# Performance work log

Hardware: AMD Instinct MI355X
Metric: run time of the kernel (lower is better)

The kernel has to match this reference:

```python
import jax, jax.numpy as jnp
import numpy as np

K = 3            # kernel_size
KK = K * K       # 9 neighbors per pixel
DILATIONS = [1, 2, 3]
NUM_HEADS = 3


def conv2d(x, w, b, dilation, padding):
    # x: [B,Cin,H,W], w: [Cout,Cin,kh,kw]
    out = jax.lax.conv_general_dilated(
        x, w, window_strides=(1, 1),
        padding=((padding, padding), (padding, padding)),
        rhs_dilation=(dilation, dilation),
        dimension_numbers=('NCHW', 'OIHW', 'NCHW'))
    if b is not None:
        out = out + b[None, :, None, None]
    return out


def unfold3(x, dil):
    # nn.Unfold(kernel=3, dilation=dil, padding=dil, stride=1): [B,C,H,W] -> [B, C*9, H*W]
    B, C, H, W = x.shape
    xp = jnp.pad(x, ((0, 0), (0, 0), (dil, dil), (dil, dil)))
    patches = [xp[:, :, i * dil:i * dil + H, j * dil:j * dil + W]
               for i in range(K) for j in range(K)]
    p = jnp.stack(patches, axis=2)          # [B,C,9,H,W] (channel-major like torch unfold)
    return p.reshape(B, C * KK, H * W)


def bilinear_sample(x, py, px):
    # x: [B,C,H,W]; py, px: [B,K2,H,W] float sample coords -> [B,C,K2,H,W]
    B, C, H, W = x.shape
    K2 = py.shape[1]
    y0 = jnp.floor(py); x0 = jnp.floor(px)
    wy = py - y0; wx = px - x0
    x_flat = x.reshape(B, C, H * W)

    def gather(yi, xi):
        yii = yi.astype(jnp.int32); xii = xi.astype(jnp.int32)
        valid = (yii >= 0) & (yii < H) & (xii >= 0) & (xii < W)
        yc = jnp.clip(yii, 0, H - 1); xc = jnp.clip(xii, 0, W - 1)
        idx = (yc * W + xc).reshape(B, -1)                       # [B, K2*H*W]
        vals = jnp.take_along_axis(x_flat, idx[:, None, :], axis=2)
        vals = vals.reshape(B, C, K2, H, W)
        return vals * valid[:, None].astype(x.dtype)

    v00 = gather(y0, x0); v01 = gather(y0, x0 + 1)
    v10 = gather(y0 + 1, x0); v11 = gather(y0 + 1, x0 + 1)
    wy = wy[:, None]; wx = wx[:, None]
    return (v00 * (1 - wy) * (1 - wx) + v01 * (1 - wy) * wx
            + v10 * wy * (1 - wx) + v11 * wy * wx)


def deform_conv(x, offsets, w, b, dil):
    # torchvision DeformConv2d, stride 1, padding=dil, dilation=dil, kernel 3
    B, C, H, W = x.shape
    off = offsets.reshape(B, KK, 2, H, W)                 # [..., (dy,dx), ...]
    ky, kx = jnp.meshgrid(jnp.arange(K), jnp.arange(K), indexing='ij')
    base_dy = (ky.reshape(KK) * dil - dil).astype(x.dtype)
    base_dx = (kx.reshape(KK) * dil - dil).astype(x.dtype)
    hh = jnp.arange(H, dtype=x.dtype); ww = jnp.arange(W, dtype=x.dtype)
    py = hh[None, None, :, None] + base_dy[None, :, None, None] + off[:, :, 0]
    px = ww[None, None, None, :] + base_dx[None, :, None, None] + off[:, :, 1]
    sampled = bilinear_sample(x, py, px)                  # [B,C,9,H,W]
    out = jnp.einsum('bckhw,ock->bohw', sampled, w.reshape(w.shape[0], C, KK))
    return out + b[None, :, None, None]


def adda_attention(q, k, v, head_dim, dil, deform_params):
    # q,k,v: [B,d,H,W] (already stop-gradiented)
    B, d, H, W = q.shape
    scale = head_dim ** -0.5
    if dil != 1:
        ow, ob, dw, db = deform_params
        offsets = conv2d(k, ow, ob, dil, dil)             # [B, 2*9, H, W]
        k = deform_conv(k, offsets, dw, db, dil)
        v = deform_conv(v, offsets, dw, db, dil)
    ku = unfold3(k, dil)                                  # [B, d*9, HW]
    vu = unfold3(v, dil)
    g = d // head_dim
    HW = H * W
    qh = q.reshape(B, g, head_dim, 1, HW).transpose(0, 1, 4, 3, 2)   # [B,g,HW,1,hd]
    kh = ku.reshape(B, g, head_dim, KK, HW).transpose(0, 1, 4, 2, 3) # [B,g,HW,hd,9]
    vh = vu.reshape(B, g, head_dim, KK, HW).transpose(0, 1, 4, 3, 2) # [B,g,HW,9,hd]
    attn = jax.nn.softmax((qh @ kh) * scale, axis=-1)                # [B,g,HW,1,9]
    o = attn @ vh                                                    # [B,g,HW,1,hd]
    return o.transpose(0, 2, 1, 3, 4).reshape(B, H, W, d)


def setup_inputs() -> dict:
    key = jax.random.key(0)
    ks = jax.random.split(key, 16)
    B, H, W, C = 8, 64, 64, 192
    hd = C // NUM_HEADS  # 64 == C // num_dilation
    inp = {
        'x': jax.random.normal(ks[0], (B, H, W, C), jnp.float32),
        'qkv_w': jax.random.normal(ks[1], (3 * C, C, 1, 1), jnp.float32) * 0.05,
        'proj_w': jax.random.normal(ks[2], (C, C), jnp.float32) * 0.05,
        'proj_b': jnp.zeros((C,), jnp.float32),
        'off_w2': jax.random.normal(ks[3], (2 * KK, hd, K, K), jnp.float32) * 0.01,
        'off_b2': jnp.zeros((2 * KK,), jnp.float32),
        'def_w2': jax.random.normal(ks[4], (hd, hd, K, K), jnp.float32) * 0.05,
        'def_b2': jnp.zeros((hd,), jnp.float32),
        'off_w3': jax.random.normal(ks[5], (2 * KK, hd, K, K), jnp.float32) * 0.01,
        'off_b3': jnp.zeros((2 * KK,), jnp.float32),
        'def_w3': jax.random.normal(ks[6], (hd, hd, K, K), jnp.float32) * 0.05,
        'def_b3': jnp.zeros((hd,), jnp.float32),
    }
    return inp


def reference(x, qkv_w, proj_w, proj_b,
              off_w2, off_b2, def_w2, def_b2,
              off_w3, off_b3, def_w3, def_b3):
    B, H, W, C = x.shape
    nd = len(DILATIONS)
    d = C // nd
    hd = C // NUM_HEADS
    xc = x.transpose(0, 3, 1, 2)                              # [B,C,H,W]
    qkv = conv2d(xc, qkv_w, None, 1, 0)                       # [B,3C,H,W]
    qkv = qkv.reshape(B, 3, nd, d, H, W).transpose(2, 1, 0, 3, 4, 5)  # [nd,3,B,d,H,W]
    qkv = jax.lax.stop_gradient(qkv)                          # q,k,v are .detach()'d in torch
    deform = {2: (off_w2, off_b2, def_w2, def_b2),
              3: (off_w3, off_b3, def_w3, def_b3)}
    outs = []
    for i, dil in enumerate(DILATIONS):
        outs.append(adda_attention(qkv[i, 0], qkv[i, 1], qkv[i, 2],
                                   hd, dil, deform.get(dil)))
    out = jnp.stack(outs, axis=3).reshape(B, H, W, C)         # permute(1,2,3,0,4).reshape
    return out @ proj_w.T + proj_b
```

## Files before the change

kernel.cpp:

```cpp
#include <hip/hip_runtime.h>
#include <cmath>

#define kB    8
#define kH    64
#define kW    64
#define kHW   4096
#define kC    192
#define kD    64
#define kM    (kB * kHW)
#define kNQKV 576

typedef unsigned short ushort_t;
typedef __attribute__((ext_vector_type(8))) short  s8v;
typedef __attribute__((ext_vector_type(4))) float  f4v;

__device__ inline unsigned short bf16r(float f) {
    union { float f; unsigned u; } v; v.f = f;
    unsigned u = v.u + 0x7FFFu + ((v.u >> 16) & 1u);
    return (unsigned short)(u >> 16);
}
__device__ inline float bfu(short s) {
    union { unsigned u; float f; } v;
    v.u = ((unsigned)(unsigned short)s) << 16;
    return v.f;
}

__global__ void cvt_bf16(const float* __restrict__ src, unsigned* __restrict__ dst, int n2) {
    int i = blockIdx.x * 256 + threadIdx.x;
    if (i >= n2) return;
    float2 f = ((const float2*)src)[i];
    dst[i] = (unsigned)bf16r(f.x) | ((unsigned)bf16r(f.y) << 16);
}

__global__ void prep_all(const float* __restrict__ qkv_w,
                         const float* __restrict__ proj_w,
                         const float* __restrict__ def_w2,
                         const float* __restrict__ def_w3,
                         const float* __restrict__ off_w2,
                         const float* __restrict__ off_w3,
                         ushort_t* __restrict__ awb,
                         ushort_t* __restrict__ pwbp,
                         ushort_t* __restrict__ dwtb2,
                         ushort_t* __restrict__ dwtb3,
                         ushort_t* __restrict__ owtb2,
                         ushort_t* __restrict__ owtb3) {
    const int bid = blockIdx.x;
    const int tid = threadIdx.x;
    if (bid < 54) {
        int idx = bid * 256 + tid;
        if (idx >= 36 * 6 * 64) return;
        int lane = idx & 63;
        int kc   = (idx >> 6) % 6;
        int s    = idx / 384;
        int row  = s * 16 + (lane & 15);
        int k0   = kc * 32 + (lane >> 4) * 8;
        const float* src = qkv_w + (size_t)row * kC + k0;
        ushort_t* dst = awb + (size_t)idx * 8;
#pragma unroll
        for (int j = 0; j < 8; ++j) dst[j] = bf16r(src[j]);
    } else if (bid < 72) {
        int idx = (bid - 54) * 256 + tid;
        if (idx >= 12 * 6 * 64) return;
        int lane = idx & 63;
        int kc   = (idx >> 6) % 6;
        int s    = idx / 384;
        int row  = s * 16 + (lane & 15);
        int k0   = kc * 32 + (lane >> 4) * 8;
        const float* src = proj_w + (size_t)row * kC + k0;
        ushort_t* dst = pwbp + (size_t)idx * 8;
#pragma unroll
        for (int j = 0; j < 8; ++j) dst[j] = bf16r(src[j]);
    } else if (bid < 360) {
        const float* dw = (bid < 216) ? def_w2 : def_w3;
        ushort_t* dwtb  = (bid < 216) ? dwtb2 : dwtb3;
        int l = ((bid < 216) ? (bid - 72) : (bid - 216)) * 256 + tid;
        if (l >= kD * kD * 9) return;
        int o = l / 576;
        int c = (l / 9) % 64;
        int kk = l % 9;
        dwtb[(kk * 64 + o) * 64 + c] = bf16r(dw[l]);
    } else {
        const float* ow = (bid < 432) ? off_w2 : off_w3;
        ushort_t* owtb  = (bid < 432) ? owtb2 : owtb3;
        int l = ((bid < 432) ? (bid - 360) : (bid - 432)) * 256 + tid;
        if (l >= 9 * 32 * 64) return;
        int kk = l >> 11;
        int j  = (l >> 6) & 31;
        int c  = l & 63;
        owtb[l] = (j < 18) ? bf16r(ow[j * 576 + c * 9 + kk]) : (ushort_t)0;
    }
}

__global__ __launch_bounds__(256) void qkv_mfma3(const ushort_t* __restrict__ xb,
                                                 const ushort_t* __restrict__ awb,
                                                 ushort_t* __restrict__ qkvpx) {
    __shared__ ushort_t xs[64 * kC];

    const int tid = threadIdx.x;
    const int bx  = blockIdx.x;
    const int lb  = (bx & 7) * 64 + (bx >> 3);
    const int m0  = lb * 64;
    const int ty3 = blockIdx.y;

#pragma unroll
    for (int i = 0; i < 6; ++i) {
        int il = i * 256 + tid;
        int p  = il / 24;
        int cc = il % 24;
        uint4 v = *(const uint4*)(xb + (size_t)(m0 + p) * kC + cc * 8);
        int dst = p * 384 + ((cc * 16) ^ ((p & 7) << 4));
        *(uint4*)((char*)xs + dst) = v;
    }
    __syncthreads();

    const int lane = tid & 63;
    const int wave = tid >> 6;
    const int l15  = lane & 15;
    const int q    = lane >> 4;
    const int sbase = ty3 * 12 + wave * 3;

    f4v acc[3][4];
#pragma unroll
    for (int i = 0; i < 3; ++i)
#pragma unroll
        for (int m = 0; m < 4; ++m) acc[i][m] = (f4v){0.f, 0.f, 0.f, 0.f};

    const ushort_t* ap = awb + ((size_t)sbase * 6 * 64 + lane) * 8;

#pragma unroll
    for (int kc = 0; kc < 6; ++kc) {
        s8v bfr[4];
#pragma unroll
        for (int m = 0; m < 4; ++m) {
            int row = m * 16 + l15;
            int col = (kc * 64 + q * 16) ^ ((l15 & 7) << 4);
            bfr[m] = *(const s8v*)((const char*)xs + row * 384 + col);
        }
#pragma unroll
        for (int i = 0; i < 3; ++i) {
            s8v a = *(const s8v*)(ap + (size_t)(i * 6 + kc) * 64 * 8);
#pragma unroll
            for (int m = 0; m < 4; ++m)
                acc[i][m] = __builtin_amdgcn_mfma_f32_16x16x32_bf16(a, bfr[m], acc[i][m], 0, 0, 0);
        }
    }

#pragma unroll
    for (int i = 0; i < 3; ++i) {
        int s   = sbase + i;
        int ty  = s >> 2;
        int c64 = (s & 3) * 16 + q * 4;
        ushort_t* obase = qkvpx + (size_t)ty * kM * 64 + (size_t)m0 * 64 + c64;
#pragma unroll
        for (int m = 0; m < 4; ++m) {
            f4v v = acc[i][m];
            uint2 u;
            u.x = (unsigned)bf16r(v.x) | ((unsigned)bf16r(v.y) << 16);
            u.y = (unsigned)bf16r(v.z) | ((unsigned)bf16r(v.w) << 16);
            *(uint2*)(obase + (size_t)(m * 16 + l15) * 64) = u;
        }
    }
}

__global__ __launch_bounds__(256) void off_conv_mfma(const ushort_t* __restrict__ kpx,
                                                     const ushort_t* __restrict__ owtb,
                                                     const float* __restrict__ obias,
                                                     float* __restrict__ offb,
                                                     int dil) {
    const int lb = (blockIdx.x & 7) * 64 + (blockIdx.x >> 3);
    const int b = lb >> 6;
    const int y = lb & 63;
    const int tid  = threadIdx.x;
    const int lane = tid & 63;
    const int wave = tid >> 6;
    const int l15  = lane & 15;
    const int q    = lane >> 4;
    const int px   = wave * 16 + l15;

    const ushort_t* inpx = kpx + (size_t)b * kHW * 64 + q * 8;

    f4v acc[2];
    acc[0] = (f4v){0.f, 0.f, 0.f, 0.f};
    acc[1] = (f4v){0.f, 0.f, 0.f, 0.f};

#pragma unroll
    for (int kk = 0; kk < 9; ++kk) {
        const int yy = y + (kk / 3 - 1) * dil;
        const int xx = px + (kk % 3 - 1) * dil;
        const bool valid = (yy >= 0) & (yy < kH) & (xx >= 0) & (xx < kW);
        const size_t idx = valid ? (size_t)(yy * kW + xx) * 64 : 0;
        s8v a0 = *(const s8v*)(inpx + idx);
        s8v a1 = *(const s8v*)(inpx + idx + 32);
        if (!valid) {
            a0 = (s8v){0, 0, 0, 0, 0, 0, 0, 0};
            a1 = (s8v){0, 0, 0, 0, 0, 0, 0, 0};
        }
        const ushort_t* wb = owtb + (size_t)kk * 2048 + l15 * 64 + q * 8;
#pragma unroll
        for (int nbk = 0; nbk < 2; ++nbk) {
            s8v b0 = *(const s8v*)(wb + nbk * 1024);
            s8v b1 = *(const s8v*)(wb + nbk * 1024 + 32);
            acc[nbk] = __builtin_amdgcn_mfma_f32_16x16x32_bf16(a0, b0, acc[nbk], 0, 0, 0);
            acc[nbk] = __builtin_amdgcn_mfma_f32_16x16x32_bf16(a1, b1, acc[nbk], 0, 0, 0);
        }
    }
#pragma unroll
    for (int nbk = 0; nbk < 2; ++nbk) {
        int n = nbk * 16 + l15;
        if (n < 18) {
            float bias = obias[n];
            f4v v = acc[nbk];
            v.x += bias; v.y += bias; v.z += bias; v.w += bias;
            *(f4v*)&offb[((size_t)b * 18 + n) * kHW + y * kW + wave * 16 + q * 4] = v;
        }
    }
}

template<int DIL>
__global__ __launch_bounds__(512) void deform_lds(const ushort_t* __restrict__ kpx,
                                                  const ushort_t* __restrict__ vpx,
                                                  const float* __restrict__ offb,
                                                  const ushort_t* __restrict__ dwtb,
                                                  const float* __restrict__ db,
                                                  ushort_t* __restrict__ outkpx,
                                                  ushort_t* __restrict__ outvpx) {
    constexpr int NR = 2 * DIL + 4;
    __shared__ ushort_t kv[NR * 4096];
    __shared__ ushort_t wlds[9 * 4096];

    const int tid = threadIdx.x;
    const int bx  = blockIdx.x;
    const int lb  = (bx & 7) * 64 + (bx >> 3);
    const int t   = lb >> 8;
    const int b   = (lb >> 5) & 7;
    const int y0  = (lb & 31) * 2;
    const int wlo = y0 - DIL - 1;

    const ushort_t* inb = (t ? vpx : kpx) + (size_t)b * kHW * 64;
    ushort_t* outp = t ? outvpx : outkpx;

#pragma unroll
    for (int i = 0; i < 9; ++i) {
        int g = (i * 512 + tid) * 16;
        uint4 v = *(const uint4*)((const char*)dwtb + g);
        int row = (g >> 7) & 63;
        int dst = g ^ ((row & 7) << 4);
        *(uint4*)((char*)wlds + dst) = v;
    }
#pragma unroll
    for (int r = 0; r < NR; ++r) {
        int gy = min(max(wlo + r, 0), kH - 1);
        uint4 v = *(const uint4*)(inb + (size_t)gy * 4096 + tid * 8);
        int x  = tid >> 3;
        int cc = tid & 7;
        int dst = r * 8192 + ((x * 128 + cc * 16) ^ ((x & 7) << 4));
        *(uint4*)((char*)kv + dst) = v;
    }
    __syncthreads();

    const int lane = tid & 63;
    const int wave = tid >> 6;
    const int ry   = wave >> 2;
    const int wc   = wave & 3;
    const int l15  = lane & 15;
    const int q    = lane >> 4;
    const int y    = y0 + ry;
    const int px   = wc * 16 + l15;
    const int wsw  = (l15 & 7) << 4;
    const int wcol0 = (q * 16) ^ wsw;
    const int wcol1 = (q * 16 + 64) ^ wsw;

    const ushort_t* inpx = inb + q * 8;

    f4v acc[4];
#pragma unroll
    for (int ob = 0; ob < 4; ++ob) acc[ob] = (f4v){0.f, 0.f, 0.f, 0.f};

    const float* offrow = offb + (size_t)b * 18 * kHW + y * kW + px;
    float offv[18];
#pragma unroll
    for (int i = 0; i < 18; ++i) offv[i] = offrow[(size_t)i * kHW];

#pragma unroll
    for (int kk = 0; kk < 9; ++kk) {
        float oy = offv[kk * 2 + 0];
        float ox = offv[kk * 2 + 1];
        float py  = (float)y  + (float)((kk / 3 - 1) * DIL) + oy;
        float pxf = (float)px + (float)((kk % 3 - 1) * DIL) + ox;
        float fy = floorf(py), fx = floorf(pxf);
        float wy = py - fy, wx = pxf - fx;
        int iy0 = (int)fy, ix0 = (int)fx;
        int iy1 = iy0 + 1, ix1 = ix0 + 1;
        int y0c = min(max(iy0, 0), kH - 1), x0c = min(max(ix0, 0), kW - 1);
        int y1c = min(max(iy1, 0), kH - 1), x1c = min(max(ix1, 0), kW - 1);
        bool vy0 = (iy0 >= 0) & (iy0 < kH), vx0 = (ix0 >= 0) & (ix0 < kW);
        bool vy1 = (iy1 >= 0) & (iy1 < kH), vx1 = (ix1 >= 0) & (ix1 < kW);
        float w0 = (vy0 && vx0) ? (1.f - wy) * (1.f - wx) : 0.f;
        float w1 = (vy0 && vx1) ? (1.f - wy) * wx : 0.f;
        float w2 = (vy1 && vx0) ? wy * (1.f - wx) : 0.f;
        float w3 = (vy1 && vx1) ? wy * wx : 0.f;

        s8v c[8];
        if (__builtin_expect(fabsf(oy) < 1.0f, 1)) {
            int r0 = min(max(y0c - wlo, 0), NR - 1);
            int r1 = min(max(y1c - wlo, 0), NR - 1);
            int b00 = r0 * 8192 + ((x0c * 128 + q * 16) ^ ((x0c & 7) << 4));
            int b00h = r0 * 8192 + ((x0c * 128 + q * 16 + 64) ^ ((x0c & 7) << 4));
            int b01 = r0 * 8192 + ((x1c * 128 + q * 16) ^ ((x1c & 7) << 4));
            int b01h = r0 * 8192 + ((x1c * 128 + q * 16 + 64) ^ ((x1c & 7) << 4));
            int b10 = r1 * 8192 + ((x0c * 128 + q * 16) ^ ((x0c & 7) << 4));
            int b10h = r1 * 8192 + ((x0c * 128 + q * 16 + 64) ^ ((x0c & 7) << 4));
            int b11 = r1 * 8192 + ((x1c * 128 + q * 16) ^ ((x1c & 7) << 4));
            int b11h = r1 * 8192 + ((x1c * 128 + q * 16 + 64) ^ ((x1c & 7) << 4));
            c[0] = *(const s8v*)((const char*)kv + b00);
            c[1] = *(const s8v*)((const char*)kv + b00h);
            c[2] = *(const s8v*)((const char*)kv + b01);
            c[3] = *(const s8v*)((const char*)kv + b01h);
            c[4] = *(const s8v*)((const char*)kv + b10);
            c[5] = *(const s8v*)((const char*)kv + b10h);
            c[6] = *(const s8v*)((const char*)kv + b11);
            c[7] = *(const s8v*)((const char*)kv + b11h);
        } else {
            size_t i00 = (size_t)(y0c * kW + x0c) * 64;
            size_t i01 = (size_t)(y0c * kW + x1c) * 64;
            size_t i10 = (size_t)(y1c * kW + x0c) * 64;
            size_t i11 = (size_t)(y1c * kW + x1c) * 64;
            c[0] = *(const s8v*)(inpx + i00);
            c[1] = *(const s8v*)(inpx + i00 + 32);
            c[2] = *(const s8v*)(inpx + i01);
            c[3] = *(const s8v*)(inpx + i01 + 32);
            c[4] = *(const s8v*)(inpx + i10);
            c[5] = *(const s8v*)(inpx + i10 + 32);
            c[6] = *(const s8v*)(inpx + i11);
            c[7] = *(const s8v*)(inpx + i11 + 32);
        }

        s8v b0, b1;
#pragma unroll
        for (int j = 0; j < 8; ++j) {
            float v0 = w0 * bfu(c[0][j]) + w1 * bfu(c[2][j]) +
                       w2 * bfu(c[4][j]) + w3 * bfu(c[6][j]);
            float v1 = w0 * bfu(c[1][j]) + w1 * bfu(c[3][j]) +
                       w2 * bfu(c[5][j]) + w3 * bfu(c[7][j]);
            b0[j] = (short)bf16r(v0);
            b1[j] = (short)bf16r(v1);
        }
        const char* wkk = (const char*)wlds + kk * 8192 + l15 * 128;
#pragma unroll
        for (int obb = 0; obb < 4; ++obb) {
            s8v a0w = *(const s8v*)(wkk + obb * 2048 + wcol0);
            s8v a1w = *(const s8v*)(wkk + obb * 2048 + wcol1);
            acc[obb] = __builtin_amdgcn_mfma_f32_16x16x32_bf16(a0w, b0, acc[obb], 0, 0, 0);
            acc[obb] = __builtin_amdgcn_mfma_f32_16x16x32_bf16(a1w, b1, acc[obb], 0, 0, 0);
        }
    }

    ushort_t* orow = outp + ((size_t)b * kHW + y * kW + px) * 64 + q * 4;
#pragma unroll
    for (int obb = 0; obb < 4; ++obb) {
        float4 bias = *(const float4*)&db[obb * 16 + q * 4];
        f4v v = acc[obb];
        uint2 u;
        u.x = (unsigned)bf16r(v.x + bias.x) | ((unsigned)bf16r(v.y + bias.y) << 16);
        u.y = (unsigned)bf16r(v.z + bias.z) | ((unsigned)bf16r(v.w + bias.w) << 16);
        *(uint2*)(orow + obb * 16) = u;
    }
}

template<int DIL>
__global__ __launch_bounds__(512) void attn_lds(const ushort_t* __restrict__ qpx,
                                                const ushort_t* __restrict__ kpx,
                                                const ushort_t* __restrict__ vpx,
                                                ushort_t* __restrict__ aopx,
                                                int branch) {
    constexpr int NR = 2 * DIL + 2;
    __shared__ ushort_t ks[NR * 4096];
    __shared__ ushort_t vs[NR * 4096];

    const int tid = threadIdx.x;
    const int bx  = blockIdx.x;
    const int lb  = (bx & 7) * 32 + (bx >> 3);
    const int b   = lb >> 5;
    const int y0  = (lb & 31) * 2;
    const int wlo = y0 - DIL;

    const size_t pbase = (size_t)b * kHW;
    const ushort_t* kb = kpx + pbase * 64;
    const ushort_t* vb = vpx + pbase * 64;

    {
        int x  = tid >> 3;
        int cc = tid & 7;
        int dstc = (x * 128 + cc * 16) ^ ((x & 7) << 4);
#pragma unroll
        for (int r = 0; r < NR; ++r) {
            int gy = min(max(wlo + r, 0), kH - 1);
            *(uint4*)((char*)ks + r * 8192 + dstc) = *(const uint4*)(kb + (size_t)gy * 4096 + tid * 8);
            *(uint4*)((char*)vs + r * 8192 + dstc) = *(const uint4*)(vb + (size_t)gy * 4096 + tid * 8);
        }
    }
    __syncthreads();

    const int wave = tid >> 6;
    const int l    = tid & 63;
    const int ry   = wave >> 2;
    const int wc   = wave & 3;
    const int pxq  = l >> 2;
    const int cg   = l & 3;
    const int y  = y0 + ry;
    const int x_ = wc * 16 + pxq;
    const int p  = y * kW + x_;

    const ushort_t* qb = qpx + (pbase + p) * 64 + cg * 16;
    s8v q0 = *(const s8v*)qb;
    s8v q1 = *(const s8v*)(qb + 8);
    float qf[16];
#pragma unroll
    for (int j = 0; j < 8; ++j) { qf[j] = bfu(q0[j]); qf[8 + j] = bfu(q1[j]); }

    int a0s[9], a1s[9];
    float msk[9];
#pragma unroll
    for (int kk = 0; kk < 9; ++kk) {
        int dy = (kk / 3 - 1) * DIL, dx = (kk % 3 - 1) * DIL;
        int yy = y + dy, xx = x_ + dx;
        bool v = (yy >= 0) & (yy < kH) & (xx >= 0) & (xx < kW);
        msk[kk] = v ? 1.f : 0.f;
        int r  = min(max(yy - wlo, 0), NR - 1);
        int xc = min(max(xx, 0), kW - 1);
        int sw = (xc & 7) << 4;
        a0s[kk] = r * 8192 + ((xc * 128 + cg * 32) ^ sw);
        a1s[kk] = r * 8192 + ((xc * 128 + cg * 32 + 16) ^ sw);
    }

    float e[9];
#pragma unroll
    for (int kk = 0; kk < 9; ++kk) {
        s8v k0 = *(const s8v*)((const char*)ks + a0s[kk]);
        s8v k1 = *(const s8v*)((const char*)ks + a1s[kk]);
        float s = 0.f;
#pragma unroll
        for (int j = 0; j < 8; ++j) {
            s += qf[j] * bfu(k0[j]);
            s += qf[8 + j] * bfu(k1[j]);
        }
        s += __shfl_xor(s, 1);
        s += __shfl_xor(s, 2);
        e[kk] = s * 0.125f * msk[kk];
    }
    float mx = -1e30f;
#pragma unroll
    for (int kk = 0; kk < 9; ++kk) mx = fmaxf(mx, e[kk]);
    float ssum = 0.f;
#pragma unroll
    for (int kk = 0; kk < 9; ++kk) { e[kk] = __expf(e[kk] - mx); ssum += e[kk]; }
    float inv = 1.f / ssum;
#pragma unroll
    for (int kk = 0; kk < 9; ++kk) e[kk] = e[kk] * inv * msk[kk];

    float acc[16];
#pragma unroll
    for (int j = 0; j < 16; ++j) acc[j] = 0.f;
#pragma unroll
    for (int kk = 0; kk < 9; ++kk) {
        s8v v0 = *(const s8v*)((const char*)vs + a0s[kk]);
        s8v v1 = *(const s8v*)((const char*)vs + a1s[kk]);
        float w = e[kk];
#pragma unroll
        for (int j = 0; j < 8; ++j) {
            acc[j] += w * bfu(v0[j]);
            acc[8 + j] += w * bfu(v1[j]);
        }
    }
    unsigned u[8];
#pragma unroll
    for (int i = 0; i < 8; ++i)
        u[i] = (unsigned)bf16r(acc[2 * i]) | ((unsigned)bf16r(acc[2 * i + 1]) << 16);
    ushort_t* ob = aopx + (pbase + p) * kC + branch * 64 + cg * 16;
    *(uint4*)ob = make_uint4(u[0], u[1], u[2], u[3]);
    *(uint4*)(ob + 8) = make_uint4(u[4], u[5], u[6], u[7]);
}

__global__ __launch_bounds__(256) void proj_mfma3(const ushort_t* __restrict__ aopx,
                                                  const ushort_t* __restrict__ pwbp,
                                                  const float* __restrict__ pb,
                                                  float* __restrict__ out) {
    __shared__ ushort_t xs[64 * kC];

    const int tid = threadIdx.x;
    const int bx  = blockIdx.x;
    const int lb  = (bx & 7) * 64 + (bx >> 3);
    const int m0  = lb * 64;

#pragma unroll
    for (int i = 0; i < 6; ++i) {
        int il = i * 256 + tid;
        int p  = il / 24;
        int cc = il % 24;
        uint4 v = *(const uint4*)(aopx + (size_t)(m0 + p) * kC + cc * 8);
        int dst = p * 384 + ((cc * 16) ^ ((p & 7) << 4));
        *(uint4*)((char*)xs + dst) = v;
    }
    __syncthreads();

    const int lane = tid & 63;
    const int wave = tid >> 6;
    const int l15  = lane & 15;
    const int q    = lane >> 4;
    const int sbase = wave * 3;

    f4v acc[3][4];
#pragma unroll
    for (int i = 0; i < 3; ++i)
#pragma unroll
        for (int m = 0; m < 4; ++m) acc[i][m] = (f4v){0.f, 0.f, 0.f, 0.f};

    const ushort_t* ap = pwbp + ((size_t)sbase * 6 * 64 + lane) * 8;

#pragma unroll
    for (int kc = 0; kc < 6; ++kc) {
        s8v bfr[4];
#pragma unroll
        for (int m = 0; m < 4; ++m) {
            int row = m * 16 + l15;
            int col = (kc * 64 + q * 16) ^ ((l15 & 7) << 4);
            bfr[m] = *(const s8v*)((const char*)xs + row * 384 + col);
        }
#pragma unroll
        for (int i = 0; i < 3; ++i) {
            s8v a = *(const s8v*)(ap + (size_t)(i * 6 + kc) * 64 * 8);
#pragma unroll
            for (int m = 0; m < 4; ++m)
                acc[i][m] = __builtin_amdgcn_mfma_f32_16x16x32_bf16(a, bfr[m], acc[i][m], 0, 0, 0);
        }
    }

#pragma unroll
    for (int i = 0; i < 3; ++i) {
        int s  = sbase + i;
        int n0 = s * 16 + q * 4;
        float4 bias = *(const float4*)&pb[n0];
#pragma unroll
        for (int m = 0; m < 4; ++m) {
            f4v v = acc[i][m];
            v.x += bias.x; v.y += bias.y; v.z += bias.z; v.w += bias.w;
            *(f4v*)&out[(size_t)(m0 + m * 16 + l15) * kC + n0] = v;
        }
    }
}

extern "C" void kernel_launch(void* const* d_in, const int* in_sizes, int n_in,
                              void* d_out, int out_size, void* d_ws, size_t ws_size,
                              hipStream_t stream) {
    const float* x      = (const float*)d_in[0];
    const float* qkv_w  = (const float*)d_in[1];
    const float* proj_w = (const float*)d_in[2];
    const float* proj_b = (const float*)d_in[3];
    const float* off_w2 = (const float*)d_in[4];
    const float* off_b2 = (const float*)d_in[5];
    const float* def_w2 = (const float*)d_in[6];
    const float* def_b2 = (const float*)d_in[7];
    const float* off_w3 = (const float*)d_in[8];
    const float* off_b3 = (const float*)d_in[9];
    const float* def_w3 = (const float*)d_in[10];
    const float* def_b3 = (const float*)d_in[11];
    float* out = (float*)d_out;

    float* ws   = (float*)d_ws;
    float* offb = ws;
    ushort_t* us = (ushort_t*)(offb + (size_t)18 * kM);
    ushort_t* xb     = us;  us += (size_t)kM * kC;
    ushort_t* qkvpx  = us;  us += (size_t)9 * kM * 64;
    ushort_t* kdpx   = us;  us += (size_t)kM * 64;
    ushort_t* vdpx   = us;  us += (size_t)kM * 64;
    ushort_t* aopx   = us;  us += (size_t)kM * kC;
    ushort_t* awb    = us;  us += (size_t)kNQKV * kC;
    ushort_t* pwbp   = us;  us += (size_t)kC * kC;
    ushort_t* dwtb2  = us;  us += kD * kD * 9;
    ushort_t* dwtb3  = us;  us += kD * kD * 9;
    ushort_t* owtb2  = us;  us += 9 * 32 * 64;
    ushort_t* owtb3  = us;  us += 9 * 32 * 64;

    cvt_bf16<<<(kM * kC / 2 + 255) / 256, 256, 0, stream>>>(x, (unsigned*)xb, kM * kC / 2);
    prep_all<<<504, 256, 0, stream>>>(qkv_w, proj_w, def_w2, def_w3, off_w2, off_w3,
                                      awb, pwbp, dwtb2, dwtb3, owtb2, owtb3);

    ushort_t* q0 = qkvpx;
    ushort_t* q1 = qkvpx + (size_t)1 * kM * 64;
    ushort_t* q2 = qkvpx + (size_t)2 * kM * 64;
    ushort_t* k0 = qkvpx + (size_t)3 * kM * 64;
    ushort_t* k1 = qkvpx + (size_t)4 * kM * 64;
    ushort_t* k2 = qkvpx + (size_t)5 * kM * 64;
    ushort_t* v0 = qkvpx + (size_t)6 * kM * 64;
    ushort_t* v1 = qkvpx + (size_t)7 * kM * 64;
    ushort_t* v2 = qkvpx + (size_t)8 * kM * 64;

    qkv_mfma3<<<dim3(kM / 64, 3), 256, 0, stream>>>(xb, awb, qkvpx);

    attn_lds<1><<<kB * kH / 2, 512, 0, stream>>>(q0, k0, v0, aopx, 0);

    off_conv_mfma<<<512, 256, 0, stream>>>(k1, owtb2, off_b2, offb, 2);
    deform_lds<2><<<512, 512, 0, stream>>>(k1, v1, offb, dwtb2, def_b2, kdpx, vdpx);
    attn_lds<2><<<kB * kH / 2, 512, 0, stream>>>(q1, kdpx, vdpx, aopx, 1);

    off_conv_mfma<<<512, 256, 0, stream>>>(k2, owtb3, off_b3, offb, 3);
    deform_lds<3><<<512, 512, 0, stream>>>(k2, v2, offb, dwtb3, def_b3, kdpx, vdpx);
    attn_lds<3><<<kB * kH / 2, 512, 0, stream>>>(q2, kdpx, vdpx, aopx, 2);

    proj_mfma3<<<512, 256, 0, stream>>>(aopx, pwbp, proj_b, out);
}
```

Before: 229.5 us.

## Batch per-dilation branches into single launches and merge conversion with weight prep

New measurement: 219.4 us. -4.4%, faster.

```diff
diff --git a/kernel.cpp b/kernel.cpp
--- a/kernel.cpp
+++ b/kernel.cpp
@@ -25,14 +25,8 @@
     return v.f;
 }
 
-__global__ void cvt_bf16(const float* __restrict__ src, unsigned* __restrict__ dst, int n2) {
-    int i = blockIdx.x * 256 + threadIdx.x;
-    if (i >= n2) return;
-    float2 f = ((const float2*)src)[i];
-    dst[i] = (unsigned)bf16r(f.x) | ((unsigned)bf16r(f.y) << 16);
-}
-
-__global__ void prep_all(const float* __restrict__ qkv_w,
+__global__ void cvt_prep(const float* __restrict__ x, unsigned* __restrict__ xb,
+                         const float* __restrict__ qkv_w,
                          const float* __restrict__ proj_w,
                          const float* __restrict__ def_w2,
                          const float* __restrict__ def_w3,
@@ -46,8 +40,13 @@
                          ushort_t* __restrict__ owtb3) {
     const int bid = blockIdx.x;
     const int tid = threadIdx.x;
-    if (bid < 54) {
-        int idx = bid * 256 + tid;
+    if (bid < 12288) {
+        int i = bid * 256 + tid;
+        if (i >= kM * kC / 2) return;
+        float2 f = ((const float2*)x)[i];
+        xb[i] = (unsigned)bf16r(f.x) | ((unsigned)bf16r(f.y) << 16);
+    } else if (bid < 12342) {
+        int idx = (bid - 12288) * 256 + tid;
         if (idx >= 36 * 6 * 64) return;
         int lane = idx & 63;
         int kc   = (idx >> 6) % 6;
@@ -58,8 +57,8 @@
         ushort_t* dst = awb + (size_t)idx * 8;
 #pragma unroll
         for (int j = 0; j < 8; ++j) dst[j] = bf16r(src[j]);
-    } else if (bid < 72) {
-        int idx = (bid - 54) * 256 + tid;
+    } else if (bid < 12360) {
+        int idx = (bid - 12342) * 256 + tid;
         if (idx >= 12 * 6 * 64) return;
         int lane = idx & 63;
         int kc   = (idx >> 6) % 6;
@@ -70,19 +69,19 @@
         ushort_t* dst = pwbp + (size_t)idx * 8;
 #pragma unroll
         for (int j = 0; j < 8; ++j) dst[j] = bf16r(src[j]);
-    } else if (bid < 360) {
-        const float* dw = (bid < 216) ? def_w2 : def_w3;
-        ushort_t* dwtb  = (bid < 216) ? dwtb2 : dwtb3;
-        int l = ((bid < 216) ? (bid - 72) : (bid - 216)) * 256 + tid;
+    } else if (bid < 12648) {
+        const float* dw = (bid < 12504) ? def_w2 : def_w3;
+        ushort_t* dwtb  = (bid < 12504) ? dwtb2 : dwtb3;
+        int l = ((bid < 12504) ? (bid - 12360) : (bid - 12504)) * 256 + tid;
         if (l >= kD * kD * 9) return;
         int o = l / 576;
         int c = (l / 9) % 64;
         int kk = l % 9;
         dwtb[(kk * 64 + o) * 64 + c] = bf16r(dw[l]);
     } else {
-        const float* ow = (bid < 432) ? off_w2 : off_w3;
-        ushort_t* owtb  = (bid < 432) ? owtb2 : owtb3;
-        int l = ((bid < 432) ? (bid - 360) : (bid - 432)) * 256 + tid;
+        const float* ow = (bid < 12720) ? off_w2 : off_w3;
+        ushort_t* owtb  = (bid < 12720) ? owtb2 : owtb3;
+        int l = ((bid < 12720) ? (bid - 12648) : (bid - 12720)) * 256 + tid;
         if (l >= 9 * 32 * 64) return;
         int kk = l >> 11;
         int j  = (l >> 6) & 31;
@@ -162,14 +161,26 @@
     }
 }
 
-__global__ __launch_bounds__(256) void off_conv_mfma(const ushort_t* __restrict__ kpx,
-                                                     const ushort_t* __restrict__ owtb,
-                                                     const float* __restrict__ obias,
-                                                     float* __restrict__ offb,
-                                                     int dil) {
-    const int lb = (blockIdx.x & 7) * 64 + (blockIdx.x >> 3);
-    const int b = lb >> 6;
-    const int y = lb & 63;
+__global__ __launch_bounds__(256) void off_conv_fused(const ushort_t* __restrict__ k1,
+                                                      const ushort_t* __restrict__ k2,
+                                                      const ushort_t* __restrict__ owtb2,
+                                                      const ushort_t* __restrict__ owtb3,
+                                                      const float* __restrict__ ob2,
+                                                      const float* __restrict__ ob3,
+                                                      float* __restrict__ offb2,
+                                                      float* __restrict__ offb3) {
+    const int bx = blockIdx.x;
+    const int lb = (bx & 7) * 128 + (bx >> 3);
+    const int zb = lb >> 9;
+    const int rest = lb & 511;
+    const int b = rest >> 6;
+    const int y = rest & 63;
+    const int dil = 2 + zb;
+    const ushort_t* kpx  = zb ? k2 : k1;
+    const ushort_t* owtb = zb ? owtb3 : owtb2;
+    const float* obias   = zb ? ob3 : ob2;
+    float* offb          = zb ? offb3 : offb2;
+
     const int tid  = threadIdx.x;
     const int lane = tid & 63;
     const int wave = tid >> 6;
@@ -216,28 +227,44 @@
     }
 }
 
-template<int DIL>
-__global__ __launch_bounds__(512) void deform_lds(const ushort_t* __restrict__ kpx,
-                                                  const ushort_t* __restrict__ vpx,
-                                                  const float* __restrict__ offb,
-                                                  const ushort_t* __restrict__ dwtb,
-                                                  const float* __restrict__ db,
-                                                  ushort_t* __restrict__ outkpx,
-                                                  ushort_t* __restrict__ outvpx) {
-    constexpr int NR = 2 * DIL + 4;
-    __shared__ ushort_t kv[NR * 4096];
+__global__ __launch_bounds__(512) void deform_fused(const ushort_t* __restrict__ k1,
+                                                    const ushort_t* __restrict__ v1,
+                                                    const ushort_t* __restrict__ k2,
+                                                    const ushort_t* __restrict__ v2,
+                                                    const float* __restrict__ offb2,
+                                                    const float* __restrict__ offb3,
+                                                    const ushort_t* __restrict__ dwtb2,
+                                                    const ushort_t* __restrict__ dwtb3,
+                                                    const float* __restrict__ db2,
+                                                    const float* __restrict__ db3,
+                                                    ushort_t* __restrict__ kd2,
+                                                    ushort_t* __restrict__ vd2,
+                                                    ushort_t* __restrict__ kd3,
+                                                    ushort_t* __restrict__ vd3) {
+    __shared__ ushort_t kv[10 * 4096];
     __shared__ ushort_t wlds[9 * 4096];
 
     const int tid = threadIdx.x;
     const int bx  = blockIdx.x;
-    const int lb  = (bx & 7) * 64 + (bx >> 3);
-    const int t   = lb >> 8;
+    const int lb  = (bx & 7) * 128 + (bx >> 3);
+    const int zb  = lb >> 9;
+    const int t   = (lb >> 8) & 1;
     const int b   = (lb >> 5) & 7;
     const int y0  = (lb & 31) * 2;
-    const int wlo = y0 - DIL - 1;
-
-    const ushort_t* inb = (t ? vpx : kpx) + (size_t)b * kHW * 64;
-    ushort_t* outp = t ? outvpx : outkpx;
+    const int dil = 2 + zb;
+    const int nr  = 2 * dil + 4;
+    const int wlo = y0 - dil - 1;
+
+    const ushort_t* kin = zb ? k2 : k1;
+    const ushort_t* vin = zb ? v2 : v1;
+    const float* offbS  = zb ? offb3 : offb2;
+    const ushort_t* dwtb = zb ? dwtb3 : dwtb2;
+    const float* db      = zb ? db3 : db2;
+    ushort_t* outk = zb ? kd3 : kd2;
+    ushort_t* outv = zb ? vd3 : vd2;
+
+    const ushort_t* inb = (t ? vin : kin) + (size_t)b * kHW * 64;
+    ushort_t* outp = t ? outv : outk;
 
 #pragma unroll
     for (int i = 0; i < 9; ++i) {
@@ -247,14 +274,15 @@
         int dst = g ^ ((row & 7) << 4);
         *(uint4*)((char*)wlds + dst) = v;
     }
-#pragma unroll
-    for (int r = 0; r < NR; ++r) {
-        int gy = min(max(wlo + r, 0), kH - 1);
-        uint4 v = *(const uint4*)(inb + (size_t)gy * 4096 + tid * 8);
+    {
         int x  = tid >> 3;
         int cc = tid & 7;
-        int dst = r * 8192 + ((x * 128 + cc * 16) ^ ((x & 7) << 4));
-        *(uint4*)((char*)kv + dst) = v;
+        int dstc = (x * 128 + cc * 16) ^ ((x & 7) << 4);
+        for (int r = 0; r < nr; ++r) {
+            int gy = min(max(wlo + r, 0), kH - 1);
+            *(uint4*)((char*)kv + r * 8192 + dstc) =
+                *(const uint4*)(inb + (size_t)gy * 4096 + tid * 8);
+        }
     }
     __syncthreads();
 
@@ -276,7 +304,7 @@
 #pragma unroll
     for (int ob = 0; ob < 4; ++ob) acc[ob] = (f4v){0.f, 0.f, 0.f, 0.f};
 
-    const float* offrow = offb + (size_t)b * 18 * kHW + y * kW + px;
+    const float* offrow = offbS + (size_t)b * 18 * kHW + y * kW + px;
     float offv[18];
 #pragma unroll
     for (int i = 0; i < 18; ++i) offv[i] = offrow[(size_t)i * kHW];
@@ -285,8 +313,8 @@
     for (int kk = 0; kk < 9; ++kk) {
         float oy = offv[kk * 2 + 0];
         float ox = offv[kk * 2 + 1];
-        float py  = (float)y  + (float)((kk / 3 - 1) * DIL) + oy;
-        float pxf = (float)px + (float)((kk % 3 - 1) * DIL) + ox;
+        float py  = (float)y  + (float)((kk / 3 - 1) * dil) + oy;
+        float pxf = (float)px + (float)((kk % 3 - 1) * dil) + ox;
         float fy = floorf(py), fx = floorf(pxf);
         float wy = py - fy, wx = pxf - fx;
         int iy0 = (int)fy, ix0 = (int)fx;
@@ -302,8 +330,8 @@
 
         s8v c[8];
         if (__builtin_expect(fabsf(oy) < 1.0f, 1)) {
-            int r0 = min(max(y0c - wlo, 0), NR - 1);
-            int r1 = min(max(y1c - wlo, 0), NR - 1);
+            int r0 = min(max(y0c - wlo, 0), nr - 1);
+            int r1 = min(max(y1c - wlo, 0), nr - 1);
             int b00 = r0 * 8192 + ((x0c * 128 + q * 16) ^ ((x0c & 7) << 4));
             int b00h = r0 * 8192 + ((x0c * 128 + q * 16 + 64) ^ ((x0c & 7) << 4));
             int b01 = r0 * 8192 + ((x1c * 128 + q * 16) ^ ((x1c & 7) << 4));
@@ -367,22 +395,33 @@
     }
 }
 
-template<int DIL>
-__global__ __launch_bounds__(512) void attn_lds(const ushort_t* __restrict__ qpx,
-                                                const ushort_t* __restrict__ kpx,
-                                                const ushort_t* __restrict__ vpx,
-                                                ushort_t* __restrict__ aopx,
-                                                int branch) {
-    constexpr int NR = 2 * DIL + 2;
-    __shared__ ushort_t ks[NR * 4096];
-    __shared__ ushort_t vs[NR * 4096];
+__global__ __launch_bounds__(512) void attn_fused(const ushort_t* __restrict__ q0,
+                                                  const ushort_t* __restrict__ k0,
+                                                  const ushort_t* __restrict__ v0,
+                                                  const ushort_t* __restrict__ q1,
+                                                  const ushort_t* __restrict__ kd2,
+                                                  const ushort_t* __restrict__ vd2,
+                                                  const ushort_t* __restrict__ q2,
+                                                  const ushort_t* __restrict__ kd3,
+                                                  const ushort_t* __restrict__ vd3,
+                                                  ushort_t* __restrict__ aopx) {
+    __shared__ ushort_t ks[8 * 4096];
+    __shared__ ushort_t vs[8 * 4096];
 
     const int tid = threadIdx.x;
     const int bx  = blockIdx.x;
-    const int lb  = (bx & 7) * 32 + (bx >> 3);
-    const int b   = lb >> 5;
-    const int y0  = (lb & 31) * 2;
-    const int wlo = y0 - DIL;
+    const int lb  = (bx & 7) * 96 + (bx >> 3);
+    const int zb  = lb >> 8;
+    const int rest = lb & 255;
+    const int b   = rest >> 5;
+    const int y0  = (rest & 31) * 2;
+    const int dil = zb + 1;
+    const int nr  = 2 * dil + 2;
+    const int wlo = y0 - dil;
+
+    const ushort_t* qpx = (zb == 0) ? q0 : (zb == 1) ? q1 : q2;
+    const ushort_t* kpx = (zb == 0) ? k0 : (zb == 1) ? kd2 : kd3;
+    const ushort_t* vpx = (zb == 0) ? v0 : (zb == 1) ? vd2 : vd3;
 
     const size_t pbase = (size_t)b * kHW;
     const ushort_t* kb = kpx + pbase * 64;
@@ -392,8 +431,7 @@
         int x  = tid >> 3;
         int cc = tid & 7;
         int dstc = (x * 128 + cc * 16) ^ ((x & 7) << 4);
-#pragma unroll
-        for (int r = 0; r < NR; ++r) {
+        for (int r = 0; r < nr; ++r) {
             int gy = min(max(wlo + r, 0), kH - 1);
             *(uint4*)((char*)ks + r * 8192 + dstc) = *(const uint4*)(kb + (size_t)gy * 4096 + tid * 8);
             *(uint4*)((char*)vs + r * 8192 + dstc) = *(const uint4*)(vb + (size_t)gy * 4096 + tid * 8);
@@ -412,21 +450,21 @@
     const int p  = y * kW + x_;
 
     const ushort_t* qb = qpx + (pbase + p) * 64 + cg * 16;
-    s8v q0 = *(const s8v*)qb;
-    s8v q1 = *(const s8v*)(qb + 8);
+    s8v qv0 = *(const s8v*)qb;
+    s8v qv1 = *(const s8v*)(qb + 8);
     float qf[16];
 #pragma unroll
-    for (int j = 0; j < 8; ++j) { qf[j] = bfu(q0[j]); qf[8 + j] = bfu(q1[j]); }
+    for (int j = 0; j < 8; ++j) { qf[j] = bfu(qv0[j]); qf[8 + j] = bfu(qv1[j]); }
 
     int a0s[9], a1s[9];
     float msk[9];
 #pragma unroll
     for (int kk = 0; kk < 9; ++kk) {
-        int dy = (kk / 3 - 1) * DIL, dx = (kk % 3 - 1) * DIL;
+        int dy = (kk / 3 - 1) * dil, dx = (kk % 3 - 1) * dil;
         int yy = y + dy, xx = x_ + dx;
         bool v = (yy >= 0) & (yy < kH) & (xx >= 0) & (xx < kW);
         msk[kk] = v ? 1.f : 0.f;
-        int r  = min(max(yy - wlo, 0), NR - 1);
+        int r  = min(max(yy - wlo, 0), nr - 1);
         int xc = min(max(xx, 0), kW - 1);
         int sw = (xc & 7) << 4;
         a0s[kk] = r * 8192 + ((xc * 128 + cg * 32) ^ sw);
@@ -436,13 +474,13 @@
     float e[9];
 #pragma unroll
     for (int kk = 0; kk < 9; ++kk) {
-        s8v k0 = *(const s8v*)((const char*)ks + a0s[kk]);
-        s8v k1 = *(const s8v*)((const char*)ks + a1s[kk]);
+        s8v k0v = *(const s8v*)((const char*)ks + a0s[kk]);
+        s8v k1v = *(const s8v*)((const char*)ks + a1s[kk]);
         float s = 0.f;
 #pragma unroll
         for (int j = 0; j < 8; ++j) {
-            s += qf[j] * bfu(k0[j]);
-            s += qf[8 + j] * bfu(k1[j]);
+            s += qf[j] * bfu(k0v[j]);
+            s += qf[8 + j] * bfu(k1v[j]);
         }
         s += __shfl_xor(s, 1);
         s += __shfl_xor(s, 2);
@@ -463,20 +501,20 @@
     for (int j = 0; j < 16; ++j) acc[j] = 0.f;
 #pragma unroll
     for (int kk = 0; kk < 9; ++kk) {
-        s8v v0 = *(const s8v*)((const char*)vs + a0s[kk]);
-        s8v v1 = *(const s8v*)((const char*)vs + a1s[kk]);
+        s8v v0v = *(const s8v*)((const char*)vs + a0s[kk]);
+        s8v v1v = *(const s8v*)((const char*)vs + a1s[kk]);
         float w = e[kk];
 #pragma unroll
         for (int j = 0; j < 8; ++j) {
-            acc[j] += w * bfu(v0[j]);
-            acc[8 + j] += w * bfu(v1[j]);
+            acc[j] += w * bfu(v0v[j]);
+            acc[8 + j] += w * bfu(v1v[j]);
         }
     }
     unsigned u[8];
 #pragma unroll
     for (int i = 0; i < 8; ++i)
         u[i] = (unsigned)bf16r(acc[2 * i]) | ((unsigned)bf16r(acc[2 * i + 1]) << 16);
-    ushort_t* ob = aopx + (pbase + p) * kC + branch * 64 + cg * 16;
+    ushort_t* ob = aopx + (pbase + p) * kC + zb * 64 + cg * 16;
     *(uint4*)ob = make_uint4(u[0], u[1], u[2], u[3]);
     *(uint4*)(ob + 8) = make_uint4(u[4], u[5], u[6], u[7]);
 }
@@ -566,13 +604,16 @@
     const float* def_b3 = (const float*)d_in[11];
     float* out = (float*)d_out;
 
-    float* ws   = (float*)d_ws;
-    float* offb = ws;
-    ushort_t* us = (ushort_t*)(offb + (size_t)18 * kM);
+    float* ws    = (float*)d_ws;
+    float* offb2 = ws;
+    float* offb3 = offb2 + (size_t)18 * kM;
+    ushort_t* us = (ushort_t*)(offb3 + (size_t)18 * kM);
     ushort_t* xb     = us;  us += (size_t)kM * kC;
     ushort_t* qkvpx  = us;  us += (size_t)9 * kM * 64;
-    ushort_t* kdpx   = us;  us += (size_t)kM * 64;
-    ushort_t* vdpx   = us;  us += (size_t)kM * 64;
+    ushort_t* kd2    = us;  us += (size_t)kM * 64;
+    ushort_t* vd2    = us;  us += (size_t)kM * 64;
+    ushort_t* kd3    = us;  us += (size_t)kM * 64;
+    ushort_t* vd3    = us;  us += (size_t)kM * 64;
     ushort_t* aopx   = us;  us += (size_t)kM * kC;
     ushort_t* awb    = us;  us += (size_t)kNQKV * kC;
     ushort_t* pwbp   = us;  us += (size_t)kC * kC;
@@ -581,9 +622,9 @@
     ushort_t* owtb2  = us;  us += 9 * 32 * 64;
     ushort_t* owtb3  = us;  us += 9 * 32 * 64;
 
-    cvt_bf16<<<(kM * kC / 2 + 255) / 256, 256, 0, stream>>>(x, (unsigned*)xb, kM * kC / 2);
-    prep_all<<<504, 256, 0, stream>>>(qkv_w, proj_w, def_w2, def_w3, off_w2, off_w3,
-                                      awb, pwbp, dwtb2, dwtb3, owtb2, owtb3);
+    cvt_prep<<<12792, 256, 0, stream>>>(x, (unsigned*)xb, qkv_w, proj_w,
+                                        def_w2, def_w3, off_w2, off_w3,
+                                        awb, pwbp, dwtb2, dwtb3, owtb2, owtb3);
 
     ushort_t* q0 = qkvpx;
     ushort_t* q1 = qkvpx + (size_t)1 * kM * 64;
@@ -597,15 +638,14 @@
 
     qkv_mfma3<<<dim3(kM / 64, 3), 256, 0, stream>>>(xb, awb, qkvpx);
 
-    attn_lds<1><<<kB * kH / 2, 512, 0, stream>>>(q0, k0, v0, aopx, 0);
-
-    off_conv_mfma<<<512, 256, 0, stream>>>(k1, owtb2, off_b2, offb, 2);
-    deform_lds<2><<<512, 512, 0, stream>>>(k1, v1, offb, dwtb2, def_b2, kdpx, vdpx);
-    attn_lds<2><<<kB * kH / 2, 512, 0, stream>>>(q1, kdpx, vdpx, aopx, 1);
-
-    off_conv_mfma<<<512, 256, 0, stream>>>(k2, owtb3, off_b3, offb, 3);
-    deform_lds<3><<<512, 512, 0, stream>>>(k2, v2, offb, dwtb3, def_b3, kdpx, vdpx);
-    attn_lds<3><<<kB * kH / 2, 512, 0, stream>>>(q2, kdpx, vdpx, aopx, 2);
+    off_conv_fused<<<1024, 256, 0, stream>>>(k1, k2, owtb2, owtb3,
+                                             off_b2, off_b3, offb2, offb3);
+
+    deform_fused<<<1024, 512, 0, stream>>>(k1, v1, k2, v2, offb2, offb3,
+                                           dwtb2, dwtb3, def_b2, def_b3,
+                                           kd2, vd2, kd3, vd3);
+
+    attn_fused<<<768, 512, 0, stream>>>(q0, k0, v0, q1, kd2, vd2, q2, kd3, vd3, aopx);
 
     proj_mfma3<<<512, 256, 0, stream>>>(aopx, pwbp, proj_b, out);
 }
```
